# Kernel optimization log

Hardware: AMD Instinct MI355X
Metric: run time of the kernel (lower is better)

Reference implementation:

```python
import jax, jax.numpy as jnp
import numpy as np

B, S, D = 2, 2048, 512
H, HD = 8, 64  # num_heads, hidden_dim; H*HD == D
FF = 2048
EPS = 1e-5


def layer_norm(x, gamma, beta):
    mu = jnp.mean(x, axis=-1, keepdims=True)
    var = jnp.mean(jnp.square(x - mu), axis=-1, keepdims=True)
    return (x - mu) * jax.lax.rsqrt(var + EPS) * gamma + beta


def setup_inputs() -> dict:
    key = jax.random.key(0)
    ks = jax.random.split(key, 16)
    s = 0.02
    return {
        "Q": jax.random.normal(ks[0], (B, S, D), jnp.float32),
        "K": jax.random.normal(ks[1], (B, S, D), jnp.float32),
        "V": jax.random.normal(ks[2], (B, S, D), jnp.float32),
        "mask": jax.random.randint(ks[3], (B, S, S), 0, 2, jnp.int32),
        "Wq": jax.random.normal(ks[4], (D, H * HD), jnp.float32) * s,
        "Wk": jax.random.normal(ks[5], (D, H * HD), jnp.float32) * s,
        "Wv": jax.random.normal(ks[6], (D, H * HD), jnp.float32) * s,
        "Wo": jax.random.normal(ks[7], (H * HD, D), jnp.float32) * s,
        "bo": jnp.zeros((D,), jnp.float32),
        "gamma": jnp.ones((D,), jnp.float32),
        "beta": jnp.zeros((D,), jnp.float32),
        "W1": jax.random.normal(ks[8], (D, FF), jnp.float32) * s,
        "b1": jnp.zeros((FF,), jnp.float32),
        "W2": jax.random.normal(ks[9], (FF, D), jnp.float32) * s,
        "b2": jnp.zeros((D,), jnp.float32),
    }


def reference(Q, K, V, mask, Wq, Wk, Wv, Wo, bo, gamma, beta, W1, b1, W2, b2):
    # NOTE: original torch code calls Z.masked_fill(...) non-inplace and drops
    # the result, so `mask` has no effect on the math. Sequence=False.
    X = V
    # Faithful (interleaving) reshape: [B, S, H*HD] -> [B*H, S, HD]
    q = (Q @ Wq).reshape(B * H, -1, HD)
    k = (K @ Wk).reshape(B * H, -1, HD)
    v = (V @ Wv).reshape(B * H, -1, HD)
    scale = jnp.sqrt(jnp.float32(D))  # sqrt(input_size[2]), not sqrt(hidden_dim)
    scores = jnp.einsum('bqd,bkd->bqk', q, k) / scale  # [B*H, S, S]
    attn = jax.nn.softmax(scores, axis=2)
    Z = jnp.einsum('bqk,bkd->bqd', attn, v)            # [B*H, S, HD]
    Z = Z.reshape(B, -1, H * HD) @ Wo + bo             # [B, S, D]
    Z = layer_norm(X + Z, gamma, beta)
    ffn = (Z @ W1 + b1) @ W2 + b2                      # no activation in source
    return layer_norm(Z + ffn, gamma, beta)
```

## Files before the change

kernel.cpp:

```cpp
#include <hip/hip_runtime.h>
#include <hip/hip_bf16.h>


typedef __hip_bfloat16 bf16;
typedef short s16x8 __attribute__((ext_vector_type(8)));
typedef short s16x4 __attribute__((ext_vector_type(4)));
typedef float f32x4 __attribute__((ext_vector_type(4)));

#if __has_builtin(__builtin_amdgcn_exp2f)
#define EXP2F(x) __builtin_amdgcn_exp2f(x)
#else
#define EXP2F(x) exp2f(x)
#endif

__device__ __forceinline__ int dtypeF32(const void* gamma) {
    return *(const unsigned int*)gamma == 0x3F800000u;
}
__device__ __forceinline__ float inElem(const void* p, size_t i, int f32) {
    return f32 ? ((const float*)p)[i]
               : __bfloat162float(((const bf16*)p)[i]);
}
__device__ __forceinline__ void outElem(void* p, size_t i, float v, int f32) {
    if (f32) ((float*)p)[i] = v;
    else     ((bf16*)p)[i] = __float2bfloat16(v);
}
__device__ __forceinline__ s16x8 load8bf(const void* p, size_t i, int f32) {
    if (f32) {
        const float* s = (const float*)p + i;
        const float4 a = *(const float4*)s;
        const float4 b = *(const float4*)(s + 4);
        bf16 t[8] = {__float2bfloat16(a.x), __float2bfloat16(a.y),
                     __float2bfloat16(a.z), __float2bfloat16(a.w),
                     __float2bfloat16(b.x), __float2bfloat16(b.y),
                     __float2bfloat16(b.z), __float2bfloat16(b.w)};
        return *(const s16x8*)t;
    }
    return *(const s16x8*)((const bf16*)p + i);
}

__device__ __forceinline__ void gll16(const bf16* g, unsigned short* l) {
    __builtin_amdgcn_global_load_lds(
        (const __attribute__((address_space(1))) unsigned int*)(const void*)g,
        (__attribute__((address_space(3))) unsigned int*)(void*)l,
        16, 0, 0);
}

__global__ __launch_bounds__(256) void tr_kernel(const void* __restrict__ s0,
                                                 const void* __restrict__ s1,
                                                 const void* __restrict__ s2,
                                                 const void* __restrict__ s3,
                                                 const void* __restrict__ s4,
                                                 bf16* __restrict__ WT4,
                                                 bf16* __restrict__ W2T,
                                                 float scale0,
                                                 const void* __restrict__ gamma) {
    const int z = blockIdx.z;
    if (z < 4 && blockIdx.y >= 16) return;
    const int f32 = dtypeF32(gamma);
    const void* src = z == 0 ? s0 : (z == 1 ? s1 : (z == 2 ? s2 : (z == 3 ? s3 : s4)));
    const int R = (z == 4) ? 2048 : 512;
    const int C = 512;
    bf16* d = (z == 4) ? W2T : WT4 + (size_t)z * 512 * 512;
    const float sc = (z == 0) ? scale0 : 1.f;
    __shared__ bf16 T[32][33];
    const int tx = threadIdx.x & 31, ty = threadIdx.x >> 5;
    const int c0 = blockIdx.x * 32, r0 = blockIdx.y * 32;
#pragma unroll
    for (int i = 0; i < 4; ++i)
        T[ty + 8 * i][tx] = __float2bfloat16(
            sc * inElem(src, (size_t)(r0 + ty + 8 * i) * C + c0 + tx, f32));
    __syncthreads();
#pragma unroll
    for (int i = 0; i < 4; ++i)
        d[(size_t)(c0 + ty + 8 * i) * R + r0 + tx] = T[tx][ty + 8 * i];
}

__global__ __launch_bounds__(64) void bc_kernel(const bf16* __restrict__ W2T,
                                                const void* __restrict__ b1,
                                                const void* __restrict__ b2,
                                                const void* __restrict__ bo,
                                                float* __restrict__ bc,
                                                float* __restrict__ bo_f,
                                                const void* __restrict__ gamma) {
    const int f32 = dtypeF32(gamma);
    const int n = blockIdx.x, lane = threadIdx.x;
    const bf16* row = W2T + (size_t)n * 2048;
    float s = 0.f;
#pragma unroll
    for (int i = 0; i < 32; ++i) {
        const int f = lane + 64 * i;
        s += inElem(b1, f, f32) * __bfloat162float(row[f]);
    }
#pragma unroll
    for (int off = 32; off; off >>= 1) s += __shfl_xor(s, off);
    if (lane == 0) {
        bc[n] = s + inElem(b2, n, f32);
        bo_f[n] = inElem(bo, n, f32);
    }
}

__global__ __launch_bounds__(256) void gemm_ks_kernel(
    const bf16* __restrict__ A, const void* __restrict__ Bt,
    float* __restrict__ Cf, const void* __restrict__ gamma) {
    __shared__ __align__(16) unsigned short As[64][40];
    __shared__ __align__(16) unsigned short Bs[128][40];

    const int bF = dtypeF32(gamma);
    const int N = 512, K = 2048, kSlice = 512;
    const int tid = threadIdx.x;
    const int w = tid >> 6, lane = tid & 63, quad = lane >> 4, l16 = lane & 15;
    const int wr = w >> 1, wc = w & 1;
    const int row0 = blockIdx.y * 64, col0 = blockIdx.x * 128;
    const int sr = tid >> 2, sc = (tid & 3) * 8;
    const int kOff = blockIdx.z * kSlice;
    float* C = Cf + (size_t)blockIdx.z * N * N;

    f32x4 acc[2][4];
#pragma unroll
    for (int rb = 0; rb < 2; ++rb)
#pragma unroll
        for (int nb = 0; nb < 4; ++nb) acc[rb][nb] = (f32x4){0.f, 0.f, 0.f, 0.f};

    for (int k0 = kOff; k0 < kOff + kSlice; k0 += 32) {
        __syncthreads();
        *(s16x8*)&As[sr][sc] = *(const s16x8*)(A + (size_t)(row0 + sr) * K + k0 + sc);
        *(s16x8*)&Bs[sr][sc] = load8bf(Bt, (size_t)(col0 + sr) * K + k0 + sc, bF);
        *(s16x8*)&Bs[sr + 64][sc] = load8bf(Bt, (size_t)(col0 + sr + 64) * K + k0 + sc, bF);
        __syncthreads();

        s16x8 aF[2], bFr[4];
#pragma unroll
        for (int rb = 0; rb < 2; ++rb)
            aF[rb] = *(const s16x8*)&As[wr * 32 + rb * 16 + l16][quad * 8];
#pragma unroll
        for (int nb = 0; nb < 4; ++nb)
            bFr[nb] = *(const s16x8*)&Bs[wc * 64 + nb * 16 + l16][quad * 8];
#pragma unroll
        for (int rb = 0; rb < 2; ++rb)
#pragma unroll
            for (int nb = 0; nb < 4; ++nb)
                acc[rb][nb] = __builtin_amdgcn_mfma_f32_16x16x32_bf16(
                    aF[rb], bFr[nb], acc[rb][nb], 0, 0, 0);
    }

#pragma unroll
    for (int rb = 0; rb < 2; ++rb)
#pragma unroll
        for (int nb = 0; nb < 4; ++nb) {
            const int col = col0 + wc * 64 + nb * 16 + l16;
#pragma unroll
            for (int r = 0; r < 4; ++r) {
                const int row = row0 + wr * 32 + rb * 16 + quad * 4 + r;
                C[(size_t)row * N + col] = acc[rb][nb][r];
            }
        }
}

__global__ __launch_bounds__(256) void combine4_kernel(const float* __restrict__ Cf,
                                                       bf16* __restrict__ WcT) {
    const int i0 = (blockIdx.x * 256 + threadIdx.x) * 4;
    const int MN = 512 * 512;
#pragma unroll
    for (int j = 0; j < 4; ++j) {
        const int i = i0 + j;
        WcT[i] = __float2bfloat16(Cf[i] + Cf[i + MN] + Cf[i + 2 * MN] + Cf[i + 3 * MN]);
    }
}

__global__ __launch_bounds__(256) void gemm_qkv_kernel(
    const void* __restrict__ Q, const void* __restrict__ K,
    const void* __restrict__ V,
    const bf16* __restrict__ WT4, bf16* __restrict__ Cbase,
    const void* __restrict__ gamma) {
    __shared__ __align__(16) unsigned short As[64][40];
    __shared__ __align__(16) unsigned short Bs[256][40];

    const int aF = dtypeF32(gamma);
    const int z = blockIdx.z;
    const void* A = z == 0 ? Q : (z == 1 ? K : V);
    const bf16* Bt = WT4 + (size_t)z * 512 * 512;
    bf16* C = Cbase + (size_t)z * 4096 * 512;

    const int tid = threadIdx.x;
    const int w = tid >> 6, lane = tid & 63, quad = lane >> 4, l16 = lane & 15;
    const int wr = w >> 1, wc = w & 1;
    const int row0 = blockIdx.y * 64, col0 = blockIdx.x * 256;
    const int sr = tid >> 2, sc = (tid & 3) * 8;

    f32x4 acc[2][8];
#pragma unroll
    for (int rb = 0; rb < 2; ++rb)
#pragma unroll
        for (int nb = 0; nb < 8; ++nb) acc[rb][nb] = (f32x4){0.f, 0.f, 0.f, 0.f};

    for (int k0 = 0; k0 < 512; k0 += 32) {
        __syncthreads();
        *(s16x8*)&As[sr][sc] = load8bf(A, (size_t)(row0 + sr) * 512 + k0 + sc, aF);
#pragma unroll
        for (int i = 0; i < 4; ++i) {
            const int br = sr + 64 * i;
            *(s16x8*)&Bs[br][sc] = *(const s16x8*)(Bt + (size_t)(col0 + br) * 512 + k0 + sc);
        }
        __syncthreads();

        s16x8 aFr[2];
#pragma unroll
        for (int rb = 0; rb < 2; ++rb)
            aFr[rb] = *(const s16x8*)&As[wr * 32 + rb * 16 + l16][quad * 8];
#pragma unroll
        for (int nb = 0; nb < 8; ++nb) {
            const s16x8 bFr = *(const s16x8*)&Bs[wc * 128 + nb * 16 + l16][quad * 8];
#pragma unroll
            for (int rb = 0; rb < 2; ++rb)
                acc[rb][nb] = __builtin_amdgcn_mfma_f32_16x16x32_bf16(
                    aFr[rb], bFr, acc[rb][nb], 0, 0, 0);
        }
    }

#pragma unroll
    for (int rb = 0; rb < 2; ++rb)
#pragma unroll
        for (int nb = 0; nb < 8; ++nb) {
            const int col = col0 + wc * 128 + nb * 16 + l16;
#pragma unroll
            for (int r = 0; r < 4; ++r) {
                const int row = row0 + wr * 32 + rb * 16 + quad * 4 + r;
                C[(size_t)row * 512 + col] = __float2bfloat16(acc[rb][nb][r]);
            }
        }
}

__global__ __launch_bounds__(256) void pack_kernel(const bf16* __restrict__ Kp,
                                                   const bf16* __restrict__ Vp,
                                                   bf16* __restrict__ KF,
                                                   bf16* __restrict__ VF) {
    const int b = blockIdx.x;
    if (b < 1024) {
        const int fid = b * 256 + threadIdx.x;
        const int lane = fid & 63, l16 = lane & 15, quad = lane >> 4;
        const int ks = (fid >> 6) & 1;
        const int jb = (fid >> 7) & 127;
        const int g = fid >> 14;
        const bf16* src = Kp + ((size_t)g * 2048 + jb * 16 + l16) * 64 + ks * 32 + quad * 8;
        *(s16x8*)(KF + (size_t)fid * 8) = *(const s16x8*)src;
    } else {
        const int fid = (b - 1024) * 256 + threadIdx.x;
        const int lane = fid & 63, l16 = lane & 15, quad = lane >> 4;
        const int db = (fid >> 6) & 3;
        const int jb = (fid >> 8) & 127;
        const int g = fid >> 15;
        bf16 t[4];
#pragma unroll
        for (int r = 0; r < 4; ++r)
            t[r] = Vp[((size_t)g * 2048 + jb * 16 + quad * 4 + r) * 64 + db * 16 + l16];
        *(s16x4*)(VF + (size_t)fid * 4) = *(const s16x4*)t;
    }
}

__global__ __launch_bounds__(256) void attn_mfma_kernel(const bf16* __restrict__ Qp,
                                                        const bf16* __restrict__ KF,
                                                        const bf16* __restrict__ VF,
                                                        bf16* __restrict__ Z) {
    const int SG = 2048;
    __shared__ __align__(16) unsigned short KsF[2][8192];
    __shared__ __align__(16) unsigned short VsF[2][8192];

    const int tid = threadIdx.x;
    const int w = tid >> 6;
    const int lane = tid & 63;
    const int quad = lane >> 4;
    const int l16 = lane & 15;

    const int g = blockIdx.x & 15;
    const int qt = blockIdx.x >> 4;
    const int qrow = g * SG + qt * 64 + w * 16 + l16;

    s16x8 bQ[2];
#pragma unroll
    for (int ks = 0; ks < 2; ++ks)
        bQ[ks] = *(const s16x8*)(Qp + (size_t)qrow * 64 + ks * 32 + quad * 8);

    f32x4 o[4];
#pragma unroll
    for (int db = 0; db < 4; ++db) o[db] = (f32x4){0.f, 0.f, 0.f, 0.f};
    f32x4 oSum = (f32x4){0.f, 0.f, 0.f, 0.f};
    const s16x4 aOnes = {(short)0x3F80, (short)0x3F80, (short)0x3F80, (short)0x3F80};

    const bf16* KFg = KF + (size_t)g * 131072;
    const bf16* VFg = VF + (size_t)g * 131072;

#pragma unroll
    for (int c = 0; c < 4; ++c) {
        const int idx = c * 256 + tid;
        gll16(KFg + (size_t)idx * 8, &KsF[0][idx * 8]);
        gll16(VFg + (size_t)idx * 8, &VsF[0][idx * 8]);
    }
    __syncthreads();

    for (int t = 0; t < 16; ++t) {
        const int cur = t & 1, nxt = cur ^ 1;
        if (t < 15) {
            const bf16* kt = KFg + (size_t)(t + 1) * 8192;
            const bf16* vt = VFg + (size_t)(t + 1) * 8192;
#pragma unroll
            for (int c = 0; c < 4; ++c) {
                const int idx = c * 256 + tid;
                gll16(kt + (size_t)idx * 8, &KsF[nxt][idx * 8]);
                gll16(vt + (size_t)idx * 8, &VsF[nxt][idx * 8]);
            }
        }

#pragma unroll
        for (int h = 0; h < 2; ++h) {
            const unsigned short* Kh = &KsF[cur][h * 4096];
            const unsigned short* Vh = &VsF[cur][h * 4096];

            f32x4 st[4];
#pragma unroll
            for (int kb = 0; kb < 4; ++kb) st[kb] = (f32x4){0.f, 0.f, 0.f, 0.f};
#pragma unroll
            for (int kb = 0; kb < 4; ++kb)
#pragma unroll
                for (int ks = 0; ks < 2; ++ks) {
                    const s16x8 aK = *(const s16x8*)&Kh[((kb * 2 + ks) * 64 + lane) * 8];
                    st[kb] = __builtin_amdgcn_mfma_f32_16x16x32_bf16(aK, bQ[ks], st[kb], 0, 0, 0);
                }

            s16x4 bP[4];
#pragma unroll
            for (int kb = 0; kb < 4; ++kb) {
                const float p0 = EXP2F(st[kb][0]);
                const float p1 = EXP2F(st[kb][1]);
                const float p2 = EXP2F(st[kb][2]);
                const float p3 = EXP2F(st[kb][3]);
                const unsigned lo = __builtin_amdgcn_perm(
                    __builtin_bit_cast(unsigned, p1), __builtin_bit_cast(unsigned, p0), 0x07060302u);
                const unsigned hi = __builtin_amdgcn_perm(
                    __builtin_bit_cast(unsigned, p3), __builtin_bit_cast(unsigned, p2), 0x07060302u);
                union { unsigned u[2]; s16x4 v; } cvt;
                cvt.u[0] = lo; cvt.u[1] = hi;
                bP[kb] = cvt.v;
            }

#pragma unroll
            for (int kb = 0; kb < 4; ++kb) {
                oSum = __builtin_amdgcn_mfma_f32_16x16x16bf16_1k(aOnes, bP[kb], oSum, 0, 0, 0);
#pragma unroll
                for (int db = 0; db < 4; ++db) {
                    const s16x4 aV = *(const s16x4*)&Vh[((kb * 4 + db) * 64 + lane) * 4];
                    o[db] = __builtin_amdgcn_mfma_f32_16x16x16bf16_1k(aV, bP[kb], o[db], 0, 0, 0);
                }
            }
        }

        if (t < 15) __syncthreads();
    }

    const float inv = 1.f / oSum[0];
#pragma unroll
    for (int db = 0; db < 4; ++db) {
        bf16 tmp[4];
#pragma unroll
        for (int r = 0; r < 4; ++r) tmp[r] = __float2bfloat16(o[db][r] * inv);
        *(s16x4*)(Z + (size_t)qrow * 64 + db * 16 + quad * 4) = *(const s16x4*)tmp;
    }
}

__global__ __launch_bounds__(256) void gemm_bt_kernel(
    const bf16* __restrict__ A, const bf16* __restrict__ Bt,
    const float* __restrict__ bias, bf16* __restrict__ C,
    int M, int N, int K) {
    __shared__ __align__(16) unsigned short As[64][40];
    __shared__ __align__(16) unsigned short Bs[128][40];

    const int tid = threadIdx.x;
    const int w = tid >> 6, lane = tid & 63, quad = lane >> 4, l16 = lane & 15;
    const int wr = w >> 1, wc = w & 1;
    const int row0 = blockIdx.y * 64, col0 = blockIdx.x * 128;
    const int sr = tid >> 2, sc = (tid & 3) * 8;

    f32x4 acc[2][4];
#pragma unroll
    for (int rb = 0; rb < 2; ++rb)
#pragma unroll
        for (int nb = 0; nb < 4; ++nb) acc[rb][nb] = (f32x4){0.f, 0.f, 0.f, 0.f};

    for (int k0 = 0; k0 < K; k0 += 32) {
        __syncthreads();
        *(s16x8*)&As[sr][sc] = *(const s16x8*)(A + (size_t)(row0 + sr) * K + k0 + sc);
        *(s16x8*)&Bs[sr][sc] = *(const s16x8*)(Bt + (size_t)(col0 + sr) * K + k0 + sc);
        *(s16x8*)&Bs[sr + 64][sc] = *(const s16x8*)(Bt + (size_t)(col0 + sr + 64) * K + k0 + sc);
        __syncthreads();

        s16x8 aF[2], bF[4];
#pragma unroll
        for (int rb = 0; rb < 2; ++rb)
            aF[rb] = *(const s16x8*)&As[wr * 32 + rb * 16 + l16][quad * 8];
#pragma unroll
        for (int nb = 0; nb < 4; ++nb)
            bF[nb] = *(const s16x8*)&Bs[wc * 64 + nb * 16 + l16][quad * 8];
#pragma unroll
        for (int rb = 0; rb < 2; ++rb)
#pragma unroll
            for (int nb = 0; nb < 4; ++nb)
                acc[rb][nb] = __builtin_amdgcn_mfma_f32_16x16x32_bf16(
                    aF[rb], bF[nb], acc[rb][nb], 0, 0, 0);
    }

#pragma unroll
    for (int rb = 0; rb < 2; ++rb)
#pragma unroll
        for (int nb = 0; nb < 4; ++nb) {
            const int col = col0 + wc * 64 + nb * 16 + l16;
            const float bv = bias[col];
#pragma unroll
            for (int r = 0; r < 4; ++r) {
                const int row = row0 + wr * 32 + rb * 16 + quad * 4 + r;
                C[(size_t)row * N + col] = __float2bfloat16(acc[rb][nb][r] + bv);
            }
        }
}

__global__ __launch_bounds__(256) void ln_res_kernel(const void* __restrict__ X, int xMode,
                                                     const bf16* __restrict__ Zin,
                                                     const void* __restrict__ gamma,
                                                     const void* __restrict__ beta,
                                                     void* __restrict__ out, int oMode) {
    const int f = dtypeF32(gamma);
    const int xF = xMode == 2 ? f : xMode;
    const int oF = oMode == 2 ? f : oMode;
    const int row = blockIdx.x * 4 + (threadIdx.x >> 6);
    const int lane = threadIdx.x & 63;
    const size_t rb = (size_t)row * 512;

    float v[8];
    float sum = 0.f, sumsq = 0.f;
#pragma unroll
    for (int i = 0; i < 8; ++i) {
        const int c = lane + 64 * i;
        const float x = inElem(X, rb + c, xF) + __bfloat162float(Zin[rb + c]);
        v[i] = x;
        sum += x;
        sumsq += x * x;
    }
#pragma unroll
    for (int off = 32; off; off >>= 1) {
        sum += __shfl_xor(sum, off);
        sumsq += __shfl_xor(sumsq, off);
    }
    const float mu = sum * (1.f / 512.f);
    const float var = sumsq * (1.f / 512.f) - mu * mu;
    const float rs = rsqrtf(var + 1e-5f);
#pragma unroll
    for (int i = 0; i < 8; ++i) {
        const int c = lane + 64 * i;
        const float gm = inElem(gamma, c, f);
        const float bt = inElem(beta, c, f);
        outElem(out, rb + c, (v[i] - mu) * rs * gm + bt, oF);
    }
}

extern "C" void kernel_launch(void* const* d_in, const int* in_sizes, int n_in,
                              void* d_out, int out_size, void* d_ws, size_t ws_size,
                              hipStream_t stream) {
    const void* Q     = d_in[0];
    const void* K     = d_in[1];
    const void* V     = d_in[2];
    const void* Wq    = d_in[4];
    const void* Wk    = d_in[5];
    const void* Wv    = d_in[6];
    const void* Wo    = d_in[7];
    const void* bo    = d_in[8];
    const void* gamma = d_in[9];
    const void* beta  = d_in[10];
    const void* W1    = d_in[11];
    const void* b1    = d_in[12];
    const void* W2    = d_in[13];
    const void* b2    = d_in[14];

    const int M = 4096;
    const size_t NT  = (size_t)M * 512;
    const size_t WSQ = 512 * 512;
    const size_t W1N = 512 * 2048;

    const size_t NEED = 27000000;
    char* scratch = (ws_size >= NEED) ? (char*)d_ws : (char*)d_in[3];

    bf16* base = (bf16*)scratch;
    bf16* Qp  = base;
    bf16* Kp  = Qp + NT;
    bf16* Vp  = Kp + NT;
    bf16* KF  = Vp + NT;
    bf16* VF  = KF + NT;
    bf16* WT4 = VF + NT;
    bf16* W2T = WT4 + 4 * WSQ;
    bf16* WcT = W2T + W1N;
    float* bc   = (float*)(WcT + WSQ);
    float* bo_f = bc + 512;
    float* Wc32 = (float*)VF;
    bf16* Zt = Kp;
    bf16* Zo = Qp;
    bf16* Z1 = Vp;
    bf16* Fo = KF;

    const dim3 blk(256);
    const float qscale = 1.4426950408889634f * 0.044194173824159216f;

    tr_kernel<<<dim3(16, 64, 5), blk, 0, stream>>>(Wq, Wk, Wv, Wo, W2,
                                                   WT4, W2T, qscale, gamma);
    bc_kernel<<<dim3(512), dim3(64), 0, stream>>>(W2T, b1, b2, bo, bc, bo_f, gamma);

    gemm_ks_kernel<<<dim3(4, 8, 4), blk, 0, stream>>>(W2T, W1, Wc32, gamma);
    combine4_kernel<<<dim3(256), blk, 0, stream>>>(Wc32, WcT);

    gemm_qkv_kernel<<<dim3(2, 64, 3), blk, 0, stream>>>(Q, K, V, WT4, Qp, gamma);

    pack_kernel<<<dim3(3072), blk, 0, stream>>>(Kp, Vp, KF, VF);

    attn_mfma_kernel<<<dim3(512), blk, 0, stream>>>(Qp, KF, VF, Zt);

    gemm_bt_kernel<<<dim3(4, 64), blk, 0, stream>>>(Zt, WT4 + 3 * WSQ, bo_f,
                                                    Zo, M, 512, 512);
    ln_res_kernel<<<dim3(1024), blk, 0, stream>>>(V, 2, Zo, gamma, beta, Z1, 0);

    gemm_bt_kernel<<<dim3(4, 64), blk, 0, stream>>>(Z1, WcT, bc, Fo, M, 512, 512);
    ln_res_kernel<<<dim3(1024), blk, 0, stream>>>(Z1, 0, Fo, gamma, beta, d_out, 2);
}
```

Baseline: 238.1 us.

## Double-buffer GEMM tiles via direct-to-LDS loads and vectorize elementwise kernels

The QKV and bias GEMM kernels now use double-buffered LDS tiles filled with global_load_lds, so the next K-slice loads while MFMAs run on the current one, and there is one barrier per iteration instead of two. The QKV kernel also changes its warp tiling to 4x4 MFMA blocks per warp. The LayerNorm, combine and bias-contraction kernels switch to 8-wide or 4-wide vector loads and stores. The LDS rows lose their padding (40 to 32 shorts), which risks bank conflicts on the fragment reads.

New measurement: 230.2 us. -3.3%, faster.

```diff
diff --git a/kernel.cpp b/kernel.cpp
--- a/kernel.cpp
+++ b/kernel.cpp
@@ -36,6 +36,32 @@
         return *(const s16x8*)t;
     }
     return *(const s16x8*)((const bf16*)p + i);
+}
+__device__ __forceinline__ void load8f(const void* p, size_t i, int f32, float* o) {
+    if (f32) {
+        const float* s = (const float*)p + i;
+        const float4 a = *(const float4*)s;
+        const float4 b = *(const float4*)(s + 4);
+        o[0] = a.x; o[1] = a.y; o[2] = a.z; o[3] = a.w;
+        o[4] = b.x; o[5] = b.y; o[6] = b.z; o[7] = b.w;
+    } else {
+        const s16x8 v = *(const s16x8*)((const bf16*)p + i);
+#pragma unroll
+        for (int j = 0; j < 8; ++j) o[j] = __bfloat162float(((const bf16*)&v)[j]);
+    }
+}
+__device__ __forceinline__ void store8(void* p, size_t i, const float* v, int f32) {
+    if (f32) {
+        float4 a = {v[0], v[1], v[2], v[3]};
+        float4 b = {v[4], v[5], v[6], v[7]};
+        *(float4*)((float*)p + i) = a;
+        *(float4*)((float*)p + i + 4) = b;
+    } else {
+        bf16 t[8];
+#pragma unroll
+        for (int j = 0; j < 8; ++j) t[j] = __float2bfloat16(v[j]);
+        *(s16x8*)((bf16*)p + i) = *(const s16x8*)t;
+    }
 }
 
 __device__ __forceinline__ void gll16(const bf16* g, unsigned short* l) {
@@ -87,9 +113,14 @@
     const bf16* row = W2T + (size_t)n * 2048;
     float s = 0.f;
 #pragma unroll
-    for (int i = 0; i < 32; ++i) {
-        const int f = lane + 64 * i;
-        s += inElem(b1, f, f32) * __bfloat162float(row[f]);
+    for (int i = 0; i < 4; ++i) {
+        const int f = lane * 8 + 512 * i;
+        float b1v[8];
+        load8f(b1, f, f32, b1v);
+        const s16x8 r = *(const s16x8*)(row + f);
+#pragma unroll
+        for (int j = 0; j < 8; ++j)
+            s += b1v[j] * __bfloat162float(((const bf16*)&r)[j]);
     }
 #pragma unroll
     for (int off = 32; off; off >>= 1) s += __shfl_xor(s, off);
@@ -158,13 +189,17 @@
 
 __global__ __launch_bounds__(256) void combine4_kernel(const float* __restrict__ Cf,
                                                        bf16* __restrict__ WcT) {
-    const int i0 = (blockIdx.x * 256 + threadIdx.x) * 4;
+    const int i = (blockIdx.x * 256 + threadIdx.x) * 4;
     const int MN = 512 * 512;
-#pragma unroll
-    for (int j = 0; j < 4; ++j) {
-        const int i = i0 + j;
-        WcT[i] = __float2bfloat16(Cf[i] + Cf[i + MN] + Cf[i + 2 * MN] + Cf[i + 3 * MN]);
-    }
+    const float4 a = *(const float4*)(Cf + i);
+    const float4 b = *(const float4*)(Cf + i + MN);
+    const float4 c = *(const float4*)(Cf + i + 2 * MN);
+    const float4 d = *(const float4*)(Cf + i + 3 * MN);
+    bf16 t[4] = {__float2bfloat16(a.x + b.x + c.x + d.x),
+                 __float2bfloat16(a.y + b.y + c.y + d.y),
+                 __float2bfloat16(a.z + b.z + c.z + d.z),
+                 __float2bfloat16(a.w + b.w + c.w + d.w)};
+    *(s16x4*)(WcT + i) = *(const s16x4*)t;
 }
 
 __global__ __launch_bounds__(256) void gemm_qkv_kernel(
@@ -172,10 +207,10 @@
     const void* __restrict__ V,
     const bf16* __restrict__ WT4, bf16* __restrict__ Cbase,
     const void* __restrict__ gamma) {
-    __shared__ __align__(16) unsigned short As[64][40];
-    __shared__ __align__(16) unsigned short Bs[256][40];
-
-    const int aF = dtypeF32(gamma);
+    __shared__ __align__(16) unsigned short As[2][64][32];
+    __shared__ __align__(16) unsigned short Bs[2][256][32];
+
+    const int aF32 = dtypeF32(gamma);
     const int z = blockIdx.z;
     const void* A = z == 0 ? Q : (z == 1 ? K : V);
     const bf16* Bt = WT4 + (size_t)z * 512 * 512;
@@ -183,48 +218,65 @@
 
     const int tid = threadIdx.x;
     const int w = tid >> 6, lane = tid & 63, quad = lane >> 4, l16 = lane & 15;
-    const int wr = w >> 1, wc = w & 1;
     const int row0 = blockIdx.y * 64, col0 = blockIdx.x * 256;
     const int sr = tid >> 2, sc = (tid & 3) * 8;
 
-    f32x4 acc[2][8];
-#pragma unroll
-    for (int rb = 0; rb < 2; ++rb)
-#pragma unroll
-        for (int nb = 0; nb < 8; ++nb) acc[rb][nb] = (f32x4){0.f, 0.f, 0.f, 0.f};
-
-    for (int k0 = 0; k0 < 512; k0 += 32) {
-        __syncthreads();
-        *(s16x8*)&As[sr][sc] = load8bf(A, (size_t)(row0 + sr) * 512 + k0 + sc, aF);
-#pragma unroll
-        for (int i = 0; i < 4; ++i) {
-            const int br = sr + 64 * i;
-            *(s16x8*)&Bs[br][sc] = *(const s16x8*)(Bt + (size_t)(col0 + br) * 512 + k0 + sc);
-        }
-        __syncthreads();
-
-        s16x8 aFr[2];
-#pragma unroll
-        for (int rb = 0; rb < 2; ++rb)
-            aFr[rb] = *(const s16x8*)&As[wr * 32 + rb * 16 + l16][quad * 8];
-#pragma unroll
-        for (int nb = 0; nb < 8; ++nb) {
-            const s16x8 bFr = *(const s16x8*)&Bs[wc * 128 + nb * 16 + l16][quad * 8];
-#pragma unroll
-            for (int rb = 0; rb < 2; ++rb)
+    f32x4 acc[4][4];
+#pragma unroll
+    for (int rb = 0; rb < 4; ++rb)
+#pragma unroll
+        for (int nb = 0; nb < 4; ++nb) acc[rb][nb] = (f32x4){0.f, 0.f, 0.f, 0.f};
+
+    const size_t aBase = (size_t)(row0 + sr) * 512 + sc;
+    const bf16* gB = Bt + (size_t)(col0 + sr) * 512 + sc;
+
+    {
+        const s16x8 a0 = load8bf(A, aBase, aF32);
+#pragma unroll
+        for (int c = 0; c < 4; ++c)
+            gll16(gB + (size_t)c * 64 * 512, &Bs[0][c * 64 + sr][sc]);
+        *(s16x8*)&As[0][sr][sc] = a0;
+    }
+    __syncthreads();
+
+    for (int t = 0; t < 16; ++t) {
+        const int cur = t & 1, nxt = cur ^ 1;
+        s16x8 aN;
+        if (t < 15) {
+            const int k = (t + 1) * 32;
+            aN = load8bf(A, aBase + k, aF32);
+#pragma unroll
+            for (int c = 0; c < 4; ++c)
+                gll16(gB + k + (size_t)c * 64 * 512, &Bs[nxt][c * 64 + sr][sc]);
+        }
+
+        s16x8 af[4];
+#pragma unroll
+        for (int rb = 0; rb < 4; ++rb)
+            af[rb] = *(const s16x8*)&As[cur][rb * 16 + l16][quad * 8];
+#pragma unroll
+        for (int nb = 0; nb < 4; ++nb) {
+            const s16x8 bf = *(const s16x8*)&Bs[cur][w * 64 + nb * 16 + l16][quad * 8];
+#pragma unroll
+            for (int rb = 0; rb < 4; ++rb)
                 acc[rb][nb] = __builtin_amdgcn_mfma_f32_16x16x32_bf16(
-                    aFr[rb], bFr, acc[rb][nb], 0, 0, 0);
-        }
-    }
-
-#pragma unroll
-    for (int rb = 0; rb < 2; ++rb)
-#pragma unroll
-        for (int nb = 0; nb < 8; ++nb) {
-            const int col = col0 + wc * 128 + nb * 16 + l16;
+                    af[rb], bf, acc[rb][nb], 0, 0, 0);
+        }
+
+        if (t < 15) {
+            *(s16x8*)&As[nxt][sr][sc] = aN;
+            __syncthreads();
+        }
+    }
+
+#pragma unroll
+    for (int rb = 0; rb < 4; ++rb)
+#pragma unroll
+        for (int nb = 0; nb < 4; ++nb) {
+            const int col = col0 + w * 64 + nb * 16 + l16;
 #pragma unroll
             for (int r = 0; r < 4; ++r) {
-                const int row = row0 + wr * 32 + rb * 16 + quad * 4 + r;
+                const int row = row0 + rb * 16 + quad * 4 + r;
                 C[(size_t)row * 512 + col] = __float2bfloat16(acc[rb][nb][r]);
             }
         }
@@ -370,8 +422,8 @@
     const bf16* __restrict__ A, const bf16* __restrict__ Bt,
     const float* __restrict__ bias, bf16* __restrict__ C,
     int M, int N, int K) {
-    __shared__ __align__(16) unsigned short As[64][40];
-    __shared__ __align__(16) unsigned short Bs[128][40];
+    __shared__ __align__(16) unsigned short As[2][64][32];
+    __shared__ __align__(16) unsigned short Bs[2][128][32];
 
     const int tid = threadIdx.x;
     const int w = tid >> 6, lane = tid & 63, quad = lane >> 4, l16 = lane & 15;
@@ -379,32 +431,46 @@
     const int row0 = blockIdx.y * 64, col0 = blockIdx.x * 128;
     const int sr = tid >> 2, sc = (tid & 3) * 8;
 
+    const bf16* gA  = A  + (size_t)(row0 + sr) * K + sc;
+    const bf16* gB0 = Bt + (size_t)(col0 + sr) * K + sc;
+    const bf16* gB1 = Bt + (size_t)(col0 + sr + 64) * K + sc;
+
     f32x4 acc[2][4];
 #pragma unroll
     for (int rb = 0; rb < 2; ++rb)
 #pragma unroll
         for (int nb = 0; nb < 4; ++nb) acc[rb][nb] = (f32x4){0.f, 0.f, 0.f, 0.f};
 
-    for (int k0 = 0; k0 < K; k0 += 32) {
-        __syncthreads();
-        *(s16x8*)&As[sr][sc] = *(const s16x8*)(A + (size_t)(row0 + sr) * K + k0 + sc);
-        *(s16x8*)&Bs[sr][sc] = *(const s16x8*)(Bt + (size_t)(col0 + sr) * K + k0 + sc);
-        *(s16x8*)&Bs[sr + 64][sc] = *(const s16x8*)(Bt + (size_t)(col0 + sr + 64) * K + k0 + sc);
-        __syncthreads();
+    const int nst = K >> 5;
+    gll16(gA,  &As[0][sr][sc]);
+    gll16(gB0, &Bs[0][sr][sc]);
+    gll16(gB1, &Bs[0][sr + 64][sc]);
+    __syncthreads();
+
+    for (int t = 0; t < nst; ++t) {
+        const int cur = t & 1, nxt = cur ^ 1;
+        if (t + 1 < nst) {
+            const int k = (t + 1) * 32;
+            gll16(gA + k,  &As[nxt][sr][sc]);
+            gll16(gB0 + k, &Bs[nxt][sr][sc]);
+            gll16(gB1 + k, &Bs[nxt][sr + 64][sc]);
+        }
 
         s16x8 aF[2], bF[4];
 #pragma unroll
         for (int rb = 0; rb < 2; ++rb)
-            aF[rb] = *(const s16x8*)&As[wr * 32 + rb * 16 + l16][quad * 8];
+            aF[rb] = *(const s16x8*)&As[cur][wr * 32 + rb * 16 + l16][quad * 8];
 #pragma unroll
         for (int nb = 0; nb < 4; ++nb)
-            bF[nb] = *(const s16x8*)&Bs[wc * 64 + nb * 16 + l16][quad * 8];
+            bF[nb] = *(const s16x8*)&Bs[cur][wc * 64 + nb * 16 + l16][quad * 8];
 #pragma unroll
         for (int rb = 0; rb < 2; ++rb)
 #pragma unroll
             for (int nb = 0; nb < 4; ++nb)
                 acc[rb][nb] = __builtin_amdgcn_mfma_f32_16x16x32_bf16(
                     aF[rb], bF[nb], acc[rb][nb], 0, 0, 0);
+
+        if (t + 1 < nst) __syncthreads();
     }
 
 #pragma unroll
@@ -432,16 +498,17 @@
     const int row = blockIdx.x * 4 + (threadIdx.x >> 6);
     const int lane = threadIdx.x & 63;
     const size_t rb = (size_t)row * 512;
+    const int c0 = lane * 8;
 
     float v[8];
+    load8f(X, rb + c0, xF, v);
+    const s16x8 z = *(const s16x8*)(Zin + rb + c0);
     float sum = 0.f, sumsq = 0.f;
 #pragma unroll
     for (int i = 0; i < 8; ++i) {
-        const int c = lane + 64 * i;
-        const float x = inElem(X, rb + c, xF) + __bfloat162float(Zin[rb + c]);
-        v[i] = x;
-        sum += x;
-        sumsq += x * x;
+        v[i] += __bfloat162float(((const bf16*)&z)[i]);
+        sum += v[i];
+        sumsq += v[i] * v[i];
     }
 #pragma unroll
     for (int off = 32; off; off >>= 1) {
@@ -451,13 +518,12 @@
     const float mu = sum * (1.f / 512.f);
     const float var = sumsq * (1.f / 512.f) - mu * mu;
     const float rs = rsqrtf(var + 1e-5f);
-#pragma unroll
-    for (int i = 0; i < 8; ++i) {
-        const int c = lane + 64 * i;
-        const float gm = inElem(gamma, c, f);
-        const float bt = inElem(beta, c, f);
-        outElem(out, rb + c, (v[i] - mu) * rs * gm + bt, oF);
-    }
+    float g[8], bt[8], o[8];
+    load8f(gamma, c0, f, g);
+    load8f(beta, c0, f, bt);
+#pragma unroll
+    for (int i = 0; i < 8; ++i) o[i] = (v[i] - mu) * rs * g[i] + bt[i];
+    store8(out, rb + c0, o, oF);
 }
 
 extern "C" void kernel_launch(void* const* d_in, const int* in_sizes, int n_in,
```
